# Optimization experiments

Hardware: AMD Instinct MI355X
Metric: run time of the kernel (lower is better)

## Reference

```python
import jax, jax.numpy as jnp
import numpy as np
from jax import lax

WINDOW = 11
SIGMA = 1.5
CHANNELS = 3
DATA_RANGE = 1.0
WEIGHTS = (0.0448, 0.2856, 0.3001, 0.2363, 0.1333)


def _gaussian_kernel_2d(size, sigma, channels):
    x = np.arange(size, dtype=np.float32) - size // 2
    k1 = np.exp(-x ** 2 / (2 * sigma ** 2))
    k1 = k1 / k1.sum()
    k2 = np.outer(k1, k1)
    k2 = k2 / k2.sum()
    return jnp.asarray(np.tile(k2[None, None], (channels, 1, 1, 1)), dtype=jnp.float32)


def _depthwise_blur(x, kernel):
    # x: [B, G, H, W], kernel: [C, 1, kh, kw] tiled to G groups
    groups = x.shape[1]
    reps = groups // kernel.shape[0]
    k = jnp.tile(kernel, (reps, 1, 1, 1))
    return lax.conv_general_dilated(
        x, k, window_strides=(1, 1), padding='SAME',
        feature_group_count=groups,
        dimension_numbers=('NCHW', 'OIHW', 'NCHW'))


def _avg_pool2(x):
    b, c, h, w = x.shape
    return x.reshape(b, c, h // 2, 2, w // 2, 2).mean(axis=(3, 5))


def _ssim_components(pred, target, kernel):
    C1 = (0.01 * DATA_RANGE) ** 2
    C2 = (0.03 * DATA_RANGE) ** 2
    # Fuse the 5 depthwise blurs into a single grouped conv over stacked channels
    stacked = jnp.concatenate(
        [pred, target, pred * pred, target * target, pred * target], axis=1)
    blurred = _depthwise_blur(stacked, kernel)
    mu1, mu2, e_pp, e_tt, e_pt = jnp.split(blurred, 5, axis=1)
    mu1_sq = mu1 * mu1
    mu2_sq = mu2 * mu2
    mu1_mu2 = mu1 * mu2
    sigma1_sq = jnp.maximum(e_pp - mu1_sq, 0.0)
    sigma2_sq = jnp.maximum(e_tt - mu2_sq, 0.0)
    sigma12 = e_pt - mu1_mu2
    l = (2 * mu1_mu2 + C1) / (mu1_sq + mu2_sq + C1)
    cs = (2 * sigma12 + C2) / (sigma1_sq + sigma2_sq + C2)
    return l.mean(), cs.mean()


def setup_inputs() -> dict:
    key = jax.random.key(0)
    k1, k2 = jax.random.split(key)
    pred = jax.random.uniform(k1, (16, 3, 512, 512), dtype=jnp.float32)
    target = jax.random.uniform(k2, (16, 3, 512, 512), dtype=jnp.float32)
    kernel = _gaussian_kernel_2d(WINDOW, SIGMA, CHANNELS)
    return {'pred': pred, 'target': target, 'kernel': kernel}


def reference(pred, target, kernel):
    weights = jnp.asarray(WEIGHTS, dtype=pred.dtype)
    msssim = jnp.ones((1,), dtype=pred.dtype)
    n_scales = len(WEIGHTS)
    for i in range(n_scales):
        if i > 0:
            pred = _avg_pool2(pred)
            target = _avg_pool2(target)
        if pred.shape[2] < WINDOW or pred.shape[3] < WINDOW:
            break
        l, cs = _ssim_components(pred, target, kernel)
        if i == n_scales - 1:
            msssim = msssim * jnp.maximum(l, 1e-8) ** weights[i] \
                            * jnp.maximum(cs, 1e-8) ** weights[i]
        else:
            msssim = msssim * jnp.maximum(cs, 1e-8) ** weights[i]
    return msssim
```

## Files before the change

kernel.cpp:

```cpp
#include <hip/hip_runtime.h>
#include <math.h>

#define NP 48

typedef float v2f __attribute__((ext_vector_type(2)));

__device__ __forceinline__ float uniform_f(float v) {
    int i = __builtin_amdgcn_readfirstlane(__builtin_bit_cast(int, v));
    return __builtin_bit_cast(float, i);
}

__device__ __forceinline__ void ssim_scale(
        const float* __restrict__ P, const float* __restrict__ T,
        int H, int sh, int lb, int scale, int slotsel, int tid,
        const float* __restrict__ k2d, double* __restrict__ accum)
{
    float w[11];
    {
        float s = 0.f;
#pragma unroll
        for (int i = 0; i < 11; ++i) s += k2d[55 + i];
        float inv = 1.0f / s;
#pragma unroll
        for (int i = 0; i < 11; ++i) w[i] = uniform_f(k2d[55 + i] * inv);
    }

    int blocksX = (NP << sh) >> 8;
    int bxi = lb % blocksX;
    int by  = lb / blocksX;
    int g   = (bxi << 8) + tid;
    int pl  = g >> sh;
    int x   = g & (H - 1);
    int yb  = by * 32;
    int yend = yb + 32;

    int bcl = x - 5;
    bcl = bcl < 0 ? 0 : bcl;
    bcl = bcl > H - 11 ? H - 11 : bcl;
    int d = bcl - (x - 5);
    float wc[11];
#pragma unroll
    for (int j = 0; j < 11; ++j) {
        int idx = j + d;
        float val = 0.f;
#pragma unroll
        for (int i = 0; i < 11; ++i) val = (idx == i) ? w[i] : val;
        wc[j] = val;
    }

    const float* pP = P + (size_t)pl * H * H + (ptrdiff_t)(yb - 5) * H + bcl;
    const float* pT = T + (size_t)pl * H * H + (ptrdiff_t)(yb - 5) * H + bcl;

    v2f wmu[11], we[11];
    float wpt[11];
    const float C1 = 1e-4f, C2 = 9e-4f;
    float lsum = 0.f, csum = 0.f;
    int rr = yb - 5;

    for (int ch = 0; ch < 4; ++ch) {
#pragma unroll
        for (int ph = 0; ph < 11; ++ph) {
            bool live = rr < yend + 5;
            v2f a_mu = (v2f){0.f, 0.f};
            v2f a_e  = (v2f){0.f, 0.f};
            v2f a_pt = (v2f){0.f, 0.f};
            if (live && rr >= 0 && rr < H) {
#pragma unroll
                for (int j = 0; j < 11; ++j) {
                    v2f pt2 = (v2f){pP[j], pT[j]};
                    v2f wv  = (v2f){wc[j], wc[j]};
                    v2f wp2 = wv * pt2;
                    v2f ptr2 = (v2f){pt2.y, pt2.x};
                    a_mu += wp2;
                    a_e  += wp2 * pt2;
                    a_pt += wp2 * ptr2;
                }
            }
            wmu[ph] = a_mu; we[ph] = a_e;
            wpt[ph] = a_pt.x + a_pt.y;
            if (live && rr >= yb + 5) {
                v2f mu2 = (v2f){0.f, 0.f};
                v2f e2  = (v2f){0.f, 0.f};
                float ept = 0.f;
#pragma unroll
                for (int i = 0; i < 11; ++i) {
                    const int sl = (ph + 1 + i) % 11;
                    v2f wi = (v2f){w[i], w[i]};
                    mu2 += wi * wmu[sl];
                    e2  += wi * we[sl];
                    ept += w[i] * wpt[sl];
                }
                float m11 = mu2.x * mu2.x, m22 = mu2.y * mu2.y, m12 = mu2.x * mu2.y;
                float s1  = fmaxf(e2.x - m11, 0.f);
                float s2  = fmaxf(e2.y - m22, 0.f);
                float s12 = 0.5f * ept - m12;
                lsum += (2.f * m12 + C1) * __builtin_amdgcn_rcpf(m11 + m22 + C1);
                csum += (2.f * s12 + C2) * __builtin_amdgcn_rcpf(s1 + s2 + C2);
            }
            rr++; pP += H; pT += H;
        }
    }

#pragma unroll
    for (int o = 32; o > 0; o >>= 1) {
        lsum += __shfl_down(lsum, o, 64);
        csum += __shfl_down(csum, o, 64);
    }
    __shared__ float red[8];
    int wv = tid >> 6;
    if ((tid & 63) == 0) { red[2 * wv] = lsum; red[2 * wv + 1] = csum; }
    __syncthreads();
    if (tid == 0) {
        int slot = (scale * 8 + slotsel) * 2;
        atomicAdd(&accum[slot],     (double)(red[0] + red[2] + red[4] + red[6]));
        atomicAdd(&accum[slot + 1], (double)(red[1] + red[3] + red[5] + red[7]));
    }
}

__global__ __launch_bounds__(256) void k_main(
        const float* __restrict__ pred, const float* __restrict__ targ,
        float* __restrict__ p1, float* __restrict__ t1,
        float* __restrict__ p2, float* __restrict__ t2,
        float* __restrict__ p3, float* __restrict__ t3,
        float* __restrict__ p4, float* __restrict__ t4,
        const float* __restrict__ k2d, double* __restrict__ accum) {
    int b   = blockIdx.x;
    int tid = threadIdx.x;
    if (b >= 1536) {
        ssim_scale(pred, targ, 512, 9, b - 1536, 0, b & 7, tid, k2d, accum);
        return;
    }
    int pi   = b >> 4;
    int tile = b & 15;
    int pls  = pi < 48 ? pi : pi - 48;
    const float* src = (pi < 48 ? pred : targ) + (size_t)pls * 512 * 512;
    float* d1 = (pi < 48 ? p1 : t1) + (size_t)pls * 256 * 256;
    float* d2 = (pi < 48 ? p2 : t2) + (size_t)pls * 128 * 128;
    float* d3 = (pi < 48 ? p3 : t3) + (size_t)pls * 64 * 64;
    float* d4 = (pi < 48 ? p4 : t4) + (size_t)pls * 32 * 32;
    int tY = tile >> 2, tX = tile & 3;
    int ty = tid >> 4, tx = tid & 15;
    int gy0 = tY * 128 + ty * 8, gx0 = tX * 128 + tx * 8;

    float s1v[4][4];
#pragma unroll
    for (int i = 0; i < 4; ++i) {
        const float* r0 = src + (size_t)(gy0 + 2 * i) * 512 + gx0;
        const float* r1 = r0 + 512;
        float4 a0 = *(const float4*)r0, a1 = *(const float4*)(r0 + 4);
        float4 b0 = *(const float4*)r1, b1 = *(const float4*)(r1 + 4);
        s1v[i][0] = 0.25f * ((a0.x + a0.y) + (b0.x + b0.y));
        s1v[i][1] = 0.25f * ((a0.z + a0.w) + (b0.z + b0.w));
        s1v[i][2] = 0.25f * ((a1.x + a1.y) + (b1.x + b1.y));
        s1v[i][3] = 0.25f * ((a1.z + a1.w) + (b1.z + b1.w));
        *(float4*)(d1 + (size_t)(tY * 64 + ty * 4 + i) * 256 + tX * 64 + tx * 4) =
            *(float4*)s1v[i];
    }
    float s2v[2][2];
#pragma unroll
    for (int i = 0; i < 2; ++i) {
#pragma unroll
        for (int j = 0; j < 2; ++j)
            s2v[i][j] = 0.25f * ((s1v[2*i][2*j] + s1v[2*i][2*j+1]) +
                                 (s1v[2*i+1][2*j] + s1v[2*i+1][2*j+1]));
        *(float2*)(d2 + (size_t)(tY * 32 + ty * 2 + i) * 128 + tX * 32 + tx * 2) =
            *(float2*)s2v[i];
    }
    float s3 = 0.25f * ((s2v[0][0] + s2v[0][1]) + (s2v[1][0] + s2v[1][1]));
    d3[(size_t)(tY * 16 + ty) * 64 + tX * 16 + tx] = s3;
    float v1 = s3 + __shfl_xor(s3, 1, 64);
    float v2 = v1 + __shfl_xor(v1, 16, 64);
    if ((ty & 1) == 0 && (tx & 1) == 0)
        d4[(size_t)(tY * 8 + (ty >> 1)) * 32 + tX * 8 + (tx >> 1)] = 0.25f * v2;
}

__global__ __launch_bounds__(256) void k_ssim_rest(
        const float* __restrict__ p1, const float* __restrict__ t1,
        const float* __restrict__ p2, const float* __restrict__ t2,
        const float* __restrict__ p3, const float* __restrict__ t3,
        const float* __restrict__ p4, const float* __restrict__ t4,
        const float* __restrict__ k2d, double* __restrict__ accum) {
    int b   = blockIdx.x;
    int tid = threadIdx.x;
    if (b < 384)      ssim_scale(p1, t1, 256, 8, b,       1, b & 7, tid, k2d, accum);
    else if (b < 480) ssim_scale(p2, t2, 128, 7, b - 384, 2, b & 7, tid, k2d, accum);
    else if (b < 504) ssim_scale(p3, t3, 64,  6, b - 480, 3, b & 7, tid, k2d, accum);
    else              ssim_scale(p4, t4, 32,  5, b - 504, 4, b & 7, tid, k2d, accum);
}

__global__ void k_final(const double* __restrict__ accum, float* __restrict__ out) {
    if (threadIdx.x != 0 || blockIdx.x != 0) return;
    const float wts[5] = {0.0448f, 0.2856f, 0.3001f, 0.2363f, 0.1333f};
    float ms = 1.0f;
    int Hs = 512;
    for (int s = 0; s < 5; ++s) {
        double lt = 0.0, ct = 0.0;
        for (int k = 0; k < 8; ++k) {
            lt += accum[(s * 8 + k) * 2];
            ct += accum[(s * 8 + k) * 2 + 1];
        }
        float N  = 48.0f * (float)Hs * (float)Hs;
        float l  = (float)lt / N;
        float cs = fmaxf((float)ct / N, 1e-8f);
        if (s == 4) {
            l = fmaxf(l, 1e-8f);
            ms *= powf(l, wts[s]) * powf(cs, wts[s]);
        } else {
            ms *= powf(cs, wts[s]);
        }
        Hs >>= 1;
    }
    out[0] = ms;
}

extern "C" void kernel_launch(void* const* d_in, const int* in_sizes, int n_in,
                              void* d_out, int out_size, void* d_ws, size_t ws_size,
                              hipStream_t stream) {
    const float* pred = (const float*)d_in[0];
    const float* targ = (const float*)d_in[1];
    const float* kern = (const float*)d_in[2];
    float* out = (float*)d_out;

    char* ws = (char*)d_ws;
    double* accum = (double*)ws;
    size_t off = 1024;
    float* p1 = (float*)(ws + off); off += (size_t)NP * 256 * 256 * 4;
    float* t1 = (float*)(ws + off); off += (size_t)NP * 256 * 256 * 4;
    float* p2 = (float*)(ws + off); off += (size_t)NP * 128 * 128 * 4;
    float* t2 = (float*)(ws + off); off += (size_t)NP * 128 * 128 * 4;
    float* p3 = (float*)(ws + off); off += (size_t)NP * 64 * 64 * 4;
    float* t3 = (float*)(ws + off); off += (size_t)NP * 64 * 64 * 4;
    float* p4 = (float*)(ws + off); off += (size_t)NP * 32 * 32 * 4;
    float* t4 = (float*)(ws + off); off += (size_t)NP * 32 * 32 * 4;

    hipMemsetAsync(accum, 0, 640, stream);
    k_main<<<3072, 256, 0, stream>>>(pred, targ, p1, t1, p2, t2, p3, t3, p4, t4, kern, accum);
    k_ssim_rest<<<510, 256, 0, stream>>>(p1, t1, p2, t2, p3, t3, p4, t4, kern, accum);
    k_final<<<1, 1, 0, stream>>>(accum, out);
}
```

Baseline: 235.6 us.

## Enlarge SSIM row tiles, drop block reduction, fuse final combine via last-block counter

Doubles the rows per SSIM block (64 instead of 32 at the two largest scales) so fewer blocks redo the 10-row vertical halo, and reorders k_main so the full-resolution SSIM blocks are scheduled before the pooling blocks. The shared-memory block reduction and __syncthreads are replaced by per-wavefront double atomics spread across slots. The separate k_final launch is removed: k_ssim_rest counts finished wavefronts with an atomic, and the last one computes the MS-SSIM product. This saves a kernel launch and some halo work, but it adds more atomics and fewer, longer blocks, which may leave the GPU less evenly loaded.

Result: slower. 296.6 us (+25.9%).

```diff
diff --git a/kernel.cpp b/kernel.cpp
--- a/kernel.cpp
+++ b/kernel.cpp
@@ -12,8 +12,9 @@
 
 __device__ __forceinline__ void ssim_scale(
         const float* __restrict__ P, const float* __restrict__ T,
-        int H, int sh, int lb, int scale, int slotsel, int tid,
-        const float* __restrict__ k2d, double* __restrict__ accum)
+        int H, int sh, int lb, int scale, int bslot, int tid,
+        const float* __restrict__ k2d, double* __restrict__ accum,
+        int BH, int nch)
 {
     float w[11];
     {
@@ -31,8 +32,8 @@
     int g   = (bxi << 8) + tid;
     int pl  = g >> sh;
     int x   = g & (H - 1);
-    int yb  = by * 32;
-    int yend = yb + 32;
+    int yb  = by * BH;
+    int yend = yb + BH;
 
     int bcl = x - 5;
     bcl = bcl < 0 ? 0 : bcl;
@@ -57,7 +58,7 @@
     float lsum = 0.f, csum = 0.f;
     int rr = yb - 5;
 
-    for (int ch = 0; ch < 4; ++ch) {
+    for (int ch = 0; ch < nch; ++ch) {
 #pragma unroll
         for (int ph = 0; ph < 11; ++ph) {
             bool live = rr < yend + 5;
@@ -106,14 +107,10 @@
         lsum += __shfl_down(lsum, o, 64);
         csum += __shfl_down(csum, o, 64);
     }
-    __shared__ float red[8];
-    int wv = tid >> 6;
-    if ((tid & 63) == 0) { red[2 * wv] = lsum; red[2 * wv + 1] = csum; }
-    __syncthreads();
-    if (tid == 0) {
-        int slot = (scale * 8 + slotsel) * 2;
-        atomicAdd(&accum[slot],     (double)(red[0] + red[2] + red[4] + red[6]));
-        atomicAdd(&accum[slot + 1], (double)(red[1] + red[3] + red[5] + red[7]));
+    if ((tid & 63) == 0) {
+        int slot = (scale * 8 + ((bslot + (tid >> 6)) & 7)) * 2;
+        atomicAdd(&accum[slot],     (double)lsum);
+        atomicAdd(&accum[slot + 1], (double)csum);
     }
 }
 
@@ -126,12 +123,13 @@
         const float* __restrict__ k2d, double* __restrict__ accum) {
     int b   = blockIdx.x;
     int tid = threadIdx.x;
-    if (b >= 1536) {
-        ssim_scale(pred, targ, 512, 9, b - 1536, 0, b & 7, tid, k2d, accum);
+    if (b < 768) {
+        ssim_scale(pred, targ, 512, 9, b, 0, b, tid, k2d, accum, 64, 7);
         return;
     }
-    int pi   = b >> 4;
-    int tile = b & 15;
+    int pb   = b - 768;
+    int pi   = pb >> 4;
+    int tile = pb & 15;
     int pls  = pi < 48 ? pi : pi - 48;
     const float* src = (pi < 48 ? pred : targ) + (size_t)pls * 512 * 512;
     float* d1 = (pi < 48 ? p1 : t1) + (size_t)pls * 256 * 256;
@@ -179,38 +177,43 @@
         const float* __restrict__ p2, const float* __restrict__ t2,
         const float* __restrict__ p3, const float* __restrict__ t3,
         const float* __restrict__ p4, const float* __restrict__ t4,
-        const float* __restrict__ k2d, double* __restrict__ accum) {
+        const float* __restrict__ k2d, double* __restrict__ accum,
+        unsigned* __restrict__ done, float* __restrict__ out) {
     int b   = blockIdx.x;
     int tid = threadIdx.x;
-    if (b < 384)      ssim_scale(p1, t1, 256, 8, b,       1, b & 7, tid, k2d, accum);
-    else if (b < 480) ssim_scale(p2, t2, 128, 7, b - 384, 2, b & 7, tid, k2d, accum);
-    else if (b < 504) ssim_scale(p3, t3, 64,  6, b - 480, 3, b & 7, tid, k2d, accum);
-    else              ssim_scale(p4, t4, 32,  5, b - 504, 4, b & 7, tid, k2d, accum);
-}
-
-__global__ void k_final(const double* __restrict__ accum, float* __restrict__ out) {
-    if (threadIdx.x != 0 || blockIdx.x != 0) return;
-    const float wts[5] = {0.0448f, 0.2856f, 0.3001f, 0.2363f, 0.1333f};
-    float ms = 1.0f;
-    int Hs = 512;
-    for (int s = 0; s < 5; ++s) {
-        double lt = 0.0, ct = 0.0;
-        for (int k = 0; k < 8; ++k) {
-            lt += accum[(s * 8 + k) * 2];
-            ct += accum[(s * 8 + k) * 2 + 1];
+    if (b < 192)      ssim_scale(p1, t1, 256, 8, b,       1, b, tid, k2d, accum, 64, 7);
+    else if (b < 288) ssim_scale(p2, t2, 128, 7, b - 192, 2, b, tid, k2d, accum, 32, 4);
+    else if (b < 312) ssim_scale(p3, t3, 64,  6, b - 288, 3, b, tid, k2d, accum, 32, 4);
+    else              ssim_scale(p4, t4, 32,  5, b - 312, 4, b, tid, k2d, accum, 32, 4);
+
+    if ((tid & 63) == 0) {
+        __threadfence();
+        unsigned old = atomicAdd(done, 1u);
+        if (old == 1271u) {
+            __threadfence();
+            const float wts[5] = {0.0448f, 0.2856f, 0.3001f, 0.2363f, 0.1333f};
+            float ms = 1.0f;
+            int Hs = 512;
+            for (int s = 0; s < 5; ++s) {
+                double lt = 0.0, ct = 0.0;
+                for (int k = 0; k < 8; ++k) {
+                    lt += atomicAdd(&accum[(s * 8 + k) * 2],     0.0);
+                    ct += atomicAdd(&accum[(s * 8 + k) * 2 + 1], 0.0);
+                }
+                float N  = 48.0f * (float)Hs * (float)Hs;
+                float l  = (float)lt / N;
+                float cs = fmaxf((float)ct / N, 1e-8f);
+                if (s == 4) {
+                    l = fmaxf(l, 1e-8f);
+                    ms *= powf(l, wts[s]) * powf(cs, wts[s]);
+                } else {
+                    ms *= powf(cs, wts[s]);
+                }
+                Hs >>= 1;
+            }
+            out[0] = ms;
         }
-        float N  = 48.0f * (float)Hs * (float)Hs;
-        float l  = (float)lt / N;
-        float cs = fmaxf((float)ct / N, 1e-8f);
-        if (s == 4) {
-            l = fmaxf(l, 1e-8f);
-            ms *= powf(l, wts[s]) * powf(cs, wts[s]);
-        } else {
-            ms *= powf(cs, wts[s]);
-        }
-        Hs >>= 1;
-    }
-    out[0] = ms;
+    }
 }
 
 extern "C" void kernel_launch(void* const* d_in, const int* in_sizes, int n_in,
@@ -222,7 +225,8 @@
     float* out = (float*)d_out;
 
     char* ws = (char*)d_ws;
-    double* accum = (double*)ws;
+    double*   accum = (double*)ws;
+    unsigned* done  = (unsigned*)(ws + 768);
     size_t off = 1024;
     float* p1 = (float*)(ws + off); off += (size_t)NP * 256 * 256 * 4;
     float* t1 = (float*)(ws + off); off += (size_t)NP * 256 * 256 * 4;
@@ -233,8 +237,7 @@
     float* p4 = (float*)(ws + off); off += (size_t)NP * 32 * 32 * 4;
     float* t4 = (float*)(ws + off); off += (size_t)NP * 32 * 32 * 4;
 
-    hipMemsetAsync(accum, 0, 640, stream);
-    k_main<<<3072, 256, 0, stream>>>(pred, targ, p1, t1, p2, t2, p3, t3, p4, t4, kern, accum);
-    k_ssim_rest<<<510, 256, 0, stream>>>(p1, t1, p2, t2, p3, t3, p4, t4, kern, accum);
-    k_final<<<1, 1, 0, stream>>>(accum, out);
-}
+    hipMemsetAsync(ws, 0, 1024, stream);
+    k_main<<<2304, 256, 0, stream>>>(pred, targ, p1, t1, p2, t2, p3, t3, p4, t4, kern, accum);
+    k_ssim_rest<<<318, 256, 0, stream>>>(p1, t1, p2, t2, p3, t3, p4, t4, kern, accum, done, out);
+}
```
